# Kernel optimization log

Hardware: AMD Instinct MI355X
Metric: run time of the kernel (lower is better)

Reference implementation:

```python
import jax, jax.numpy as jnp
import numpy as np

B, T, D = 32, 512, 768      # batch, n_tokens, input_dim
M, K, R = 2048, 32, 128     # n_mentions, k_retrieval, retrieval_dim
H = 1024                    # hidden_dim
EPS = 1e-12


def _layer_norm(x, scale, bias, eps=EPS):
    mu = jnp.mean(x, axis=-1, keepdims=True)
    var = jnp.mean(jnp.square(x - mu), axis=-1, keepdims=True)
    return (x - mu) * jax.lax.rsqrt(var + eps) * scale + bias


def _mlp_block(x, w1, b1, w2, b2, ln_s, ln_b):
    # Dense -> gelu -> Dense -> residual -> LayerNorm (dropout off, deterministic)
    h = jax.nn.gelu(x @ w1 + b1)
    h = h @ w2 + b2
    return _layer_norm(h + x, ln_s, ln_b)


def setup_inputs() -> dict:
    key = jax.random.key(0)
    ks = jax.random.split(key, 24)
    s = lambda *sh: 1.0 / np.sqrt(sh[0])
    inp = {
        'encoded_input': jax.random.normal(ks[0], (B, T, D), jnp.float32),
        'retrieval_values': jax.random.normal(ks[1], (M, K, R), jnp.float32),
        'retrieval_scores': jax.random.uniform(ks[2], (M, K), jnp.float32),
        'mention_batch_positions': jax.random.randint(ks[3], (M,), 0, B),
        'mention_start_positions': jax.random.randint(ks[4], (M,), 0, T),
        'mention_end_positions': jax.random.randint(ks[5], (M,), 0, T),
        'mention_mask': jnp.ones((M,), jnp.float32),
        # value_projection: concat(start,end) [2D] -> R
        'vp_w': jax.random.normal(ks[6], (2 * D, R), jnp.float32) * s(2 * D),
        'vp_b': jnp.zeros((R,), jnp.float32),
        # concat_mlp: [2R] -> H ; concat_dense: H -> D
        'cm_w': jax.random.normal(ks[7], (2 * R, H), jnp.float32) * s(2 * R),
        'cm_b': jnp.zeros((H,), jnp.float32),
        'cd_w': jax.random.normal(ks[8], (H, D), jnp.float32) * s(H),
        'cd_b': jnp.zeros((D,), jnp.float32),
        # additional concat MLPBlock (1 layer)
        'ac_w1': jax.random.normal(ks[9], (D, H), jnp.float32) * s(D),
        'ac_b1': jnp.zeros((H,), jnp.float32),
        'ac_w2': jax.random.normal(ks[10], (H, D), jnp.float32) * s(H),
        'ac_b2': jnp.zeros((D,), jnp.float32),
        'ac_ln_s': jnp.ones((D,), jnp.float32),
        'ac_ln_b': jnp.zeros((D,), jnp.float32),
        # pooled MLPBlock (1 layer)
        'pl_w1': jax.random.normal(ks[11], (D, H), jnp.float32) * s(D),
        'pl_b1': jnp.zeros((H,), jnp.float32),
        'pl_w2': jax.random.normal(ks[12], (H, D), jnp.float32) * s(H),
        'pl_b2': jnp.zeros((D,), jnp.float32),
        'pl_ln_s': jnp.ones((D,), jnp.float32),
        'pl_ln_b': jnp.zeros((D,), jnp.float32),
        # final layer norm
        'ln_s': jnp.ones((D,), jnp.float32),
        'ln_b': jnp.zeros((D,), jnp.float32),
    }
    return inp


def reference(encoded_input, retrieval_values, retrieval_scores,
              mention_batch_positions, mention_start_positions,
              mention_end_positions, mention_mask,
              vp_w, vp_b, cm_w, cm_b, cd_w, cd_b,
              ac_w1, ac_b1, ac_w2, ac_b2, ac_ln_s, ac_ln_b,
              pl_w1, pl_b1, pl_w2, pl_b2, pl_ln_s, pl_ln_b,
              ln_s, ln_b):
    # gather mention start/end encodings: [M, D] each
    start_enc = encoded_input[mention_batch_positions, mention_start_positions]
    end_enc = encoded_input[mention_batch_positions, mention_end_positions]
    pmv = jnp.concatenate((start_enc, end_enc), axis=-1) @ vp_w + vp_b  # [M, R]
    # tile over retrievals and concat: [M, K, 2R]
    pmv = jnp.broadcast_to(pmv[:, None, :], (pmv.shape[0], retrieval_values.shape[1], pmv.shape[-1]))
    cv = jnp.concatenate((pmv, retrieval_values), axis=-1)
    cv = jax.nn.gelu(cv @ cm_w + cm_b)
    cv = cv @ cd_w + cd_b                                              # [M, K, D]
    cv = _mlp_block(cv, ac_w1, ac_b1, ac_w2, ac_b2, ac_ln_s, ac_ln_b)
    pooled = jnp.einsum('qk,qkd->qd', retrieval_scores, cv)            # [M, D]
    pooled = _mlp_block(pooled, pl_w1, pl_b1, pl_w2, pl_b2, pl_ln_s, pl_ln_b)
    pooled = pooled * mention_mask[:, None]
    out = encoded_input.at[mention_batch_positions, mention_start_positions].add(pooled)
    return _layer_norm(out, ln_s, ln_b)
```

## Files before the change

### kernel.cpp

```cpp
#include <hip/hip_runtime.h>
#include <hip/hip_bf16.h>

#define Bq 32
#define Tq 512
#define Dq 768
#define Mq 2048
#define Kq 32
#define Rq 128
#define Hq 1024
#define NROWS (Mq * Kq)
#define CH 32768
#define NCH (NROWS / CH)

typedef short short8 __attribute__((ext_vector_type(8)));
typedef unsigned short ushort4v __attribute__((ext_vector_type(4)));
typedef float f32x4 __attribute__((ext_vector_type(4)));

__device__ __forceinline__ unsigned short f2bf(float f) {
    union { float f; unsigned u; } v; v.f = f;
    unsigned r = v.u + 0x7FFFu + ((v.u >> 16) & 1u);
    return (unsigned short)(r >> 16);
}
__device__ __forceinline__ float bf2f(unsigned short h) {
    union { unsigned u; float f; } v; v.u = ((unsigned)h) << 16;
    return v.f;
}
__device__ __forceinline__ float gelu_f(float x) {
    float u = x * (1.5957691216057308f + 0.07135481622212034f * x * x);
    return x / (1.0f + __expf(-u));
}

__device__ __forceinline__ void block_reduce2(float& a, float& b, float* sm) {
    #pragma unroll
    for (int off = 32; off > 0; off >>= 1) {
        a += __shfl_down(a, off, 64);
        b += __shfl_down(b, off, 64);
    }
    int lane = threadIdx.x & 63, wid = threadIdx.x >> 6;
    if (lane == 0) { sm[wid * 2] = a; sm[wid * 2 + 1] = b; }
    __syncthreads();
    if (threadIdx.x == 0) {
        float sa = 0.f, sb = 0.f;
        #pragma unroll
        for (int w = 0; w < 4; ++w) { sa += sm[w * 2]; sb += sm[w * 2 + 1]; }
        sm[0] = sa; sm[1] = sb;
    }
    __syncthreads();
    a = sm[0]; b = sm[1];
    __syncthreads();
}

__global__ __launch_bounds__(256) void wtrans_k(
    const float* __restrict__ W, unsigned short* __restrict__ Wt, int K, int N)
{
    __shared__ unsigned short t[32][33];
    int n0 = blockIdx.x * 32, k0 = blockIdx.y * 32;
    int tx = threadIdx.x & 31, ty = threadIdx.x >> 5;
    #pragma unroll
    for (int i = 0; i < 32; i += 8)
        t[ty + i][tx] = f2bf(W[(long)(k0 + ty + i) * N + n0 + tx]);
    __syncthreads();
    #pragma unroll
    for (int i = 0; i < 32; i += 8)
        Wt[(long)(n0 + ty + i) * K + k0 + tx] = t[tx][ty + i];
}

__global__ __launch_bounds__(256) void rv2bf_k(
    const float* __restrict__ rv, unsigned short* __restrict__ rvb)
{
    long i = ((long)blockIdx.x * 256 + threadIdx.x) * 8;
    float4 a = *reinterpret_cast<const float4*>(rv + i);
    float4 b = *reinterpret_cast<const float4*>(rv + i + 4);
    unsigned short v[8] = {f2bf(a.x), f2bf(a.y), f2bf(a.z), f2bf(a.w),
                           f2bf(b.x), f2bf(b.y), f2bf(b.z), f2bf(b.w)};
    *(short8*)(rvb + i) = *(short8*)v;
}

__global__ __launch_bounds__(192) void gather_enc_k(
    const float* __restrict__ enc, const int* __restrict__ bpos,
    const int* __restrict__ spos, const int* __restrict__ epos,
    unsigned short* __restrict__ cat)
{
    int m = blockIdx.x;
    int t = threadIdx.x;
    int b = bpos[m];
    int pos = (t < 96) ? spos[m] : epos[m];
    int off = (t < 96) ? t * 8 : (t - 96) * 8;
    const float4* s = reinterpret_cast<const float4*>(enc + ((long)b * Tq + pos) * Dq + off);
    float4 a = s[0], c = s[1];
    unsigned short v[8] = {f2bf(a.x), f2bf(a.y), f2bf(a.z), f2bf(a.w),
                           f2bf(c.x), f2bf(c.y), f2bf(c.z), f2bf(c.w)};
    *(short8*)(cat + (long)m * 1536 + t * 8) = *(short8*)v;
}

template <int ACT, int OUT_BF16, int RESID, int CONCAT>
__global__ __launch_bounds__(256) void mgemm_k(
    const unsigned short* __restrict__ A,
    const unsigned short* __restrict__ Wt,
    const float* __restrict__ bias,
    void* __restrict__ Cout,
    const unsigned short* __restrict__ resid,
    int Kd, int N,
    const unsigned short* __restrict__ pmvb,
    const unsigned short* __restrict__ rvb,
    int row_base)
{
    __shared__ __align__(16) unsigned short AsLin[2][128 * 32];
    __shared__ __align__(16) unsigned short BsLin[2][128 * 32];
    const int tid = threadIdx.x;
    const int w = tid >> 6, lane = tid & 63;
    const int wr = w >> 1, wc = w & 1;
    const int lr = lane & 15, lk = lane >> 4;
    const long r0 = (long)blockIdx.x * 128;
    const int c0 = blockIdx.y * 128;
    const int nt = Kd >> 5;

    auto stage = [&](int buf, int t) {
        const int k0 = t << 5;
        #pragma unroll
        for (int cc = 0; cc < 2; ++cc) {
            int idx = (w * 2 + cc) * 64 + lane;
            int row = idx >> 2, kc = idx & 3;
            int kcol = k0 + kc * 8;
            const unsigned short* ga;
            if (CONCAT) {
                long gr = row_base + r0 + row;
                ga = (kcol < 128) ? pmvb + ((gr >> 5) << 7) + kcol
                                  : rvb + (gr << 7) + (kcol - 128);
            } else {
                ga = A + (r0 + row) * Kd + kcol;
            }
            __builtin_amdgcn_global_load_lds(
                (const __attribute__((address_space(1))) void*)ga,
                (__attribute__((address_space(3))) void*)(&AsLin[buf][(w * 2 + cc) * 512]),
                16, 0, 0);
            const unsigned short* gb = Wt + (long)(c0 + row) * Kd + kcol;
            __builtin_amdgcn_global_load_lds(
                (const __attribute__((address_space(1))) void*)gb,
                (__attribute__((address_space(3))) void*)(&BsLin[buf][(w * 2 + cc) * 512]),
                16, 0, 0);
        }
    };

    f32x4 acc[4][4] = {};

    stage(0, 0);
    if (nt > 1) stage(1, 1);

    for (int t = 0; t < nt; ++t) {
        const int cur = t & 1;
        if (t + 1 < nt) asm volatile("s_waitcnt vmcnt(4)" ::: "memory");
        else            asm volatile("s_waitcnt vmcnt(0)" ::: "memory");
        asm volatile("s_barrier" ::: "memory");

        short8 af[4], bv[4];
        #pragma unroll
        for (int m = 0; m < 4; ++m)
            af[m] = *(const short8*)(&AsLin[cur][(wr * 64 + m * 16 + lr) * 32 + lk * 8]);
        #pragma unroll
        for (int n = 0; n < 4; ++n)
            bv[n] = *(const short8*)(&BsLin[cur][(wc * 64 + n * 16 + lr) * 32 + lk * 8]);

        asm volatile("s_waitcnt lgkmcnt(0)" ::: "memory");
        asm volatile("s_barrier" ::: "memory");

        if (t + 2 < nt) stage(cur, t + 2);

        #pragma unroll
        for (int m = 0; m < 4; ++m)
            #pragma unroll
            for (int n = 0; n < 4; ++n)
                acc[m][n] = __builtin_amdgcn_mfma_f32_16x16x32_bf16(
                    af[m], bv[n], acc[m][n], 0, 0, 0);
    }

    const int cb = c0 + wc * 64;
    #pragma unroll
    for (int n = 0; n < 4; ++n) {
        const int c = cb + n * 16 + lr;
        const float bc = bias[c];
        #pragma unroll
        for (int m = 0; m < 4; ++m) {
            const long r = r0 + wr * 64 + m * 16 + lk * 4;
            #pragma unroll
            for (int j = 0; j < 4; ++j) {
                float v = acc[m][n][j] + bc;
                if (ACT) v = gelu_f(v);
                if (RESID) v += bf2f(resid[(r + j) * N + c]);
                if (OUT_BF16) ((unsigned short*)Cout)[(r + j) * N + c] = f2bf(v);
                else          ((float*)Cout)[(r + j) * N + c] = v;
            }
        }
    }
}

template <int ACT, int OUT_BF16, int RESID, int CONCAT, int NF>
__global__ __launch_bounds__(512, 2) void mgemm256_k(
    const unsigned short* __restrict__ A,
    const unsigned short* __restrict__ Wt,
    const float* __restrict__ bias,
    void* __restrict__ Cout,
    const unsigned short* __restrict__ resid,
    int Kd, int N,
    const unsigned short* __restrict__ pmvb,
    const unsigned short* __restrict__ rvb,
    int row_base)
{
    __shared__ __align__(16) unsigned short As[2][256 * 32];
    __shared__ __align__(16) unsigned short Bs[2][NF * 64 * 32];
    const int tid = threadIdx.x;
    const int w = tid >> 6, lane = tid & 63;
    const int wr = w >> 2, wc = w & 3;
    const int lr = lane & 15, lk = lane >> 4;
    const long r0 = (long)blockIdx.x * 256;
    const int c0 = blockIdx.y * (NF * 64);
    const int nt = Kd >> 5;
    const int wb = (NF == 4) ? w : (w >= 6 ? w - 6 : w);

    auto stage = [&](int buf, int t) {
        const int k0 = t << 5;
        #pragma unroll
        for (int q = 0; q < 2; ++q) {
            int ca = w * 128 + q * 64 + lane;
            int rowa = ca >> 2, kca = ca & 3;
            int kcol = k0 + kca * 8;
            const unsigned short* ga;
            if (CONCAT) {
                long gr = row_base + r0 + rowa;
                ga = (kcol < 128) ? pmvb + ((gr >> 5) << 7) + kcol
                                  : rvb + (gr << 7) + (kcol - 128);
            } else {
                ga = A + (r0 + rowa) * Kd + kcol;
            }
            __builtin_amdgcn_global_load_lds(
                (const __attribute__((address_space(1))) void*)ga,
                (__attribute__((address_space(3))) void*)(&As[buf][(w * 128 + q * 64) * 8]),
                16, 0, 0);
            int cb_ = wb * 128 + q * 64 + lane;
            int rowb = cb_ >> 2, kcb = cb_ & 3;
            const unsigned short* gb = Wt + (long)(c0 + rowb) * Kd + k0 + kcb * 8;
            __builtin_amdgcn_global_load_lds(
                (const __attribute__((address_space(1))) void*)gb,
                (__attribute__((address_space(3))) void*)(&Bs[buf][(wb * 128 + q * 64) * 8]),
                16, 0, 0);
        }
    };

    f32x4 acc[8][NF] = {};

    stage(0, 0);
    if (nt > 1) stage(1, 1);

    for (int t = 0; t < nt; ++t) {
        const int cur = t & 1;
        if (t + 1 < nt) asm volatile("s_waitcnt vmcnt(4)" ::: "memory");
        else            asm volatile("s_waitcnt vmcnt(0)" ::: "memory");
        asm volatile("s_barrier" ::: "memory");

        short8 af[8], bv[NF];
        #pragma unroll
        for (int m = 0; m < 8; ++m)
            af[m] = *(const short8*)(&As[cur][(wr * 128 + m * 16 + lr) * 32 + lk * 8]);
        #pragma unroll
        for (int n = 0; n < NF; ++n)
            bv[n] = *(const short8*)(&Bs[cur][(wc * (NF * 16) + n * 16 + lr) * 32 + lk * 8]);

        asm volatile("s_waitcnt lgkmcnt(0)" ::: "memory");
        asm volatile("s_barrier" ::: "memory");

        if (t + 2 < nt) stage(cur, t + 2);

        #pragma unroll
        for (int m = 0; m < 8; ++m)
            #pragma unroll
            for (int n = 0; n < NF; ++n)
                acc[m][n] = __builtin_amdgcn_mfma_f32_16x16x32_bf16(
                    af[m], bv[n], acc[m][n], 0, 0, 0);
    }

    const int cb = c0 + wc * (NF * 16);
    #pragma unroll
    for (int n = 0; n < NF; ++n) {
        const int c = cb + n * 16 + lr;
        const float bc = bias[c];
        #pragma unroll
        for (int m = 0; m < 8; ++m) {
            const long r = r0 + wr * 128 + m * 16 + lk * 4;
            #pragma unroll
            for (int j = 0; j < 4; ++j) {
                float v = acc[m][n][j] + bc;
                if (ACT) v = gelu_f(v);
                if (RESID) v += bf2f(resid[(r + j) * N + c]);
                if (OUT_BF16) ((unsigned short*)Cout)[(r + j) * N + c] = f2bf(v);
                else          ((float*)Cout)[(r + j) * N + c] = v;
            }
        }
    }
}

__global__ __launch_bounds__(512) void ln_pool_part_k(
    const unsigned short* __restrict__ cvb, const float* __restrict__ scores,
    const float* __restrict__ ln_s, const float* __restrict__ ln_b,
    float* __restrict__ partial,
    int mbase)
{
    __shared__ float part[8][768];
    int lm = blockIdx.x >> 2, ks = blockIdx.x & 3;
    int gm = mbase + lm;
    int tid = threadIdx.x, lane = tid & 63, wid = tid >> 6;
    int k = ks * 8 + wid;
    const unsigned short* row = cvb + ((long)lm * 32 + k) * Dq;

    float v[12], gs[12], gb[12];
    float s = 0.f, ss = 0.f;
    #pragma unroll
    for (int j = 0; j < 3; ++j) {
        int col = j * 256 + lane * 4;
        ushort4v u = *(const ushort4v*)(row + col);
        float4 g = *reinterpret_cast<const float4*>(ln_s + col);
        float4 h = *reinterpret_cast<const float4*>(ln_b + col);
        #pragma unroll
        for (int t = 0; t < 4; ++t) {
            float x = bf2f(u[t]);
            v[j * 4 + t] = x;
            s += x; ss += x * x;
        }
        gs[j * 4 + 0] = g.x; gs[j * 4 + 1] = g.y; gs[j * 4 + 2] = g.z; gs[j * 4 + 3] = g.w;
        gb[j * 4 + 0] = h.x; gb[j * 4 + 1] = h.y; gb[j * 4 + 2] = h.z; gb[j * 4 + 3] = h.w;
    }
    #pragma unroll
    for (int off = 32; off > 0; off >>= 1) {
        s  += __shfl_xor(s, off, 64);
        ss += __shfl_xor(ss, off, 64);
    }
    float mu = s * (1.0f / Dq);
    float var = ss * (1.0f / Dq) - mu * mu;
    float rstd = rsqrtf(var + 1e-12f);
    float sc = scores[gm * 32 + k];
    #pragma unroll
    for (int j = 0; j < 3; ++j) {
        int col = j * 256 + lane * 4;
        #pragma unroll
        for (int t = 0; t < 4; ++t)
            part[wid][col + t] = sc * ((v[j * 4 + t] - mu) * rstd * gs[j * 4 + t] + gb[j * 4 + t]);
    }
    __syncthreads();
    for (int d = tid; d < Dq; d += 512) {
        float acc = 0.f;
        #pragma unroll
        for (int w = 0; w < 8; ++w) acc += part[w][d];
        partial[((long)lm * 4 + ks) * Dq + d] = acc;
    }
}

__global__ __launch_bounds__(256) void ln_pool_comb_k(
    const float* __restrict__ partial, float* __restrict__ pooledf,
    unsigned short* __restrict__ pooledb, int mbase)
{
    int lm = blockIdx.x, gm = mbase + lm;
    int tid = threadIdx.x;
    for (int d = tid; d < Dq; d += 256) {
        const float* p = partial + (long)lm * 4 * Dq + d;
        float s = p[0] + p[Dq] + p[2 * Dq] + p[3 * Dq];
        pooledf[(long)gm * Dq + d] = s;
        pooledb[(long)gm * Dq + d] = f2bf(s);
    }
}

__global__ __launch_bounds__(256) void ln_mask_scatter_k(
    const float* __restrict__ pu, const float* __restrict__ pooled,
    const float* __restrict__ ln_s, const float* __restrict__ ln_b,
    const float* __restrict__ mask,
    const int* __restrict__ bpos, const int* __restrict__ spos,
    float* __restrict__ out)
{
    __shared__ float sm[8];
    int m = blockIdx.x;
    int tid = threadIdx.x;
    float v[3];
    float s = 0.f, ss = 0.f;
    #pragma unroll
    for (int j = 0; j < 3; ++j) {
        int d = tid + j * 256;
        v[j] = pu[(long)m * Dq + d] + pooled[(long)m * Dq + d];
        s += v[j]; ss += v[j] * v[j];
    }
    block_reduce2(s, ss, sm);
    float mu = s * (1.0f / Dq);
    float var = ss * (1.0f / Dq) - mu * mu;
    float rstd = rsqrtf(var + 1e-12f);
    float mk = mask[m];
    long orow = ((long)bpos[m] * Tq + spos[m]) * Dq;
    #pragma unroll
    for (int j = 0; j < 3; ++j) {
        int d = tid + j * 256;
        float y = ((v[j] - mu) * rstd * ln_s[d] + ln_b[d]) * mk;
        atomicAdd(&out[orow + d], y);
    }
}

__global__ __launch_bounds__(256) void final_ln_k(
    float* __restrict__ out, const float* __restrict__ ln_s,
    const float* __restrict__ ln_b)
{
    __shared__ float sm[8];
    int tid = threadIdx.x;
    float* row = out + (long)blockIdx.x * Dq;
    float v[3];
    float s = 0.f, ss = 0.f;
    #pragma unroll
    for (int j = 0; j < 3; ++j) {
        v[j] = row[tid + j * 256];
        s += v[j]; ss += v[j] * v[j];
    }
    block_reduce2(s, ss, sm);
    float mu = s * (1.0f / Dq);
    float var = ss * (1.0f / Dq) - mu * mu;
    float rstd = rsqrtf(var + 1e-12f);
    #pragma unroll
    for (int j = 0; j < 3; ++j) {
        int d = tid + j * 256;
        row[d] = (v[j] - mu) * rstd * ln_s[d] + ln_b[d];
    }
}

extern "C" void kernel_launch(void* const* d_in, const int* in_sizes, int n_in,
                              void* d_out, int out_size, void* d_ws, size_t ws_size,
                              hipStream_t stream) {
    const float* enc    = (const float*)d_in[0];
    const float* rv     = (const float*)d_in[1];
    const float* scores = (const float*)d_in[2];
    const int*   bpos   = (const int*)d_in[3];
    const int*   spos   = (const int*)d_in[4];
    const int*   epos   = (const int*)d_in[5];
    const float* mask   = (const float*)d_in[6];
    const float* vp_w   = (const float*)d_in[7];
    const float* vp_b   = (const float*)d_in[8];
    const float* cm_w   = (const float*)d_in[9];
    const float* cm_b   = (const float*)d_in[10];
    const float* cd_w   = (const float*)d_in[11];
    const float* cd_b   = (const float*)d_in[12];
    const float* ac_w1  = (const float*)d_in[13];
    const float* ac_b1  = (const float*)d_in[14];
    const float* ac_w2  = (const float*)d_in[15];
    const float* ac_b2  = (const float*)d_in[16];
    const float* ac_ln_s = (const float*)d_in[17];
    const float* ac_ln_b = (const float*)d_in[18];
    const float* pl_w1  = (const float*)d_in[19];
    const float* pl_b1  = (const float*)d_in[20];
    const float* pl_w2  = (const float*)d_in[21];
    const float* pl_b2  = (const float*)d_in[22];
    const float* pl_ln_s = (const float*)d_in[23];
    const float* pl_ln_b = (const float*)d_in[24];
    const float* ln_s   = (const float*)d_in[25];
    const float* ln_b   = (const float*)d_in[26];
    float* out = (float*)d_out;

    char* wsb = (char*)d_ws;
    unsigned short* wt_cm = (unsigned short*)wsb; wsb += (size_t)1024 * 256 * 2;
    unsigned short* wt_cd = (unsigned short*)wsb; wsb += (size_t)768 * 1024 * 2;
    unsigned short* wt_a1 = (unsigned short*)wsb; wsb += (size_t)1024 * 768 * 2;
    unsigned short* wt_a2 = (unsigned short*)wsb; wsb += (size_t)768 * 1024 * 2;
    unsigned short* wt_p1 = (unsigned short*)wsb; wsb += (size_t)1024 * 768 * 2;
    unsigned short* wt_p2 = (unsigned short*)wsb; wsb += (size_t)768 * 1024 * 2;
    unsigned short* wt_vp = (unsigned short*)wsb; wsb += (size_t)128 * 1536 * 2;
    unsigned short* pmvb  = (unsigned short*)wsb; wsb += (size_t)Mq * Rq * 2;
    unsigned short* rvb   = (unsigned short*)wsb; wsb += (size_t)NROWS * Rq * 2;
    unsigned short* catenc = (unsigned short*)wsb; wsb += (size_t)Mq * 1536 * 2;
    unsigned short* hb    = (unsigned short*)wsb; wsb += (size_t)CH * Hq * 2;
    unsigned short* tb    = (unsigned short*)wsb; wsb += (size_t)CH * Dq * 2;
    unsigned short* cvb   = (unsigned short*)wsb; wsb += (size_t)CH * Dq * 2;
    float* partial = (float*)wsb; wsb += (size_t)(CH / Kq) * 4 * Dq * 4;
    float* pooledf = (float*)wsb; wsb += (size_t)Mq * Dq * 4;
    unsigned short* pooledb = (unsigned short*)wsb; wsb += (size_t)Mq * Dq * 2;
    float* puf     = (float*)wsb; wsb += (size_t)Mq * Dq * 4;

    hipMemcpyAsync(out, enc, (size_t)Bq * Tq * Dq * sizeof(float),
                   hipMemcpyDeviceToDevice, stream);

    wtrans_k<<<dim3(1024 / 32, 256 / 32), 256, 0, stream>>>(cm_w, wt_cm, 256, 1024);
    wtrans_k<<<dim3(768 / 32, 1024 / 32), 256, 0, stream>>>(cd_w, wt_cd, 1024, 768);
    wtrans_k<<<dim3(1024 / 32, 768 / 32), 256, 0, stream>>>(ac_w1, wt_a1, 768, 1024);
    wtrans_k<<<dim3(768 / 32, 1024 / 32), 256, 0, stream>>>(ac_w2, wt_a2, 1024, 768);
    wtrans_k<<<dim3(1024 / 32, 768 / 32), 256, 0, stream>>>(pl_w1, wt_p1, 768, 1024);
    wtrans_k<<<dim3(768 / 32, 1024 / 32), 256, 0, stream>>>(pl_w2, wt_p2, 1024, 768);
    wtrans_k<<<dim3(128 / 32, 1536 / 32), 256, 0, stream>>>(vp_w, wt_vp, 1536, 128);
    rv2bf_k<<<(NROWS * Rq) / (256 * 8), 256, 0, stream>>>(rv, rvb);

    gather_enc_k<<<Mq, 192, 0, stream>>>(enc, bpos, spos, epos, catenc);
    mgemm_k<0, 1, 0, 0><<<dim3(Mq / 128, 1), 256, 0, stream>>>(
        catenc, wt_vp, vp_b, pmvb, nullptr, 1536, Rq, nullptr, nullptr, 0);

    for (int c = 0; c < NCH; ++c) {
        int row_base = c * CH;
        int mbase = c * (CH / Kq);
        mgemm256_k<1, 1, 0, 1, 4><<<dim3(CH / 256, Hq / 256), 512, 0, stream>>>(
            nullptr, wt_cm, cm_b, hb, nullptr, 2 * Rq, Hq, pmvb, rvb, row_base);
        mgemm256_k<0, 1, 0, 0, 3><<<dim3(CH / 256, Dq / 192), 512, 0, stream>>>(
            hb, wt_cd, cd_b, tb, nullptr, Hq, Dq, nullptr, nullptr, 0);
        mgemm256_k<1, 1, 0, 0, 4><<<dim3(CH / 256, Hq / 256), 512, 0, stream>>>(
            tb, wt_a1, ac_b1, hb, nullptr, Dq, Hq, nullptr, nullptr, 0);
        mgemm256_k<0, 1, 1, 0, 3><<<dim3(CH / 256, Dq / 192), 512, 0, stream>>>(
            hb, wt_a2, ac_b2, cvb, tb, Hq, Dq, nullptr, nullptr, 0);
        ln_pool_part_k<<<(CH / Kq) * 4, 512, 0, stream>>>(
            cvb, scores, ac_ln_s, ac_ln_b, partial, mbase);
        ln_pool_comb_k<<<CH / Kq, 256, 0, stream>>>(partial, pooledf, pooledb, mbase);
    }

    mgemm_k<1, 1, 0, 0><<<dim3(Mq / 128, Hq / 128), 256, 0, stream>>>(
        pooledb, wt_p1, pl_b1, hb, nullptr, Dq, Hq, nullptr, nullptr, 0);
    mgemm_k<0, 0, 0, 0><<<dim3(Mq / 128, Dq / 128), 256, 0, stream>>>(
        hb, wt_p2, pl_b2, puf, nullptr, Hq, Dq, nullptr, nullptr, 0);

    ln_mask_scatter_k<<<Mq, 256, 0, stream>>>(puf, pooledf, pl_ln_s, pl_ln_b,
                                              mask, bpos, spos, out);

    final_ln_k<<<Bq * Tq, 256, 0, stream>>>(out, ln_s, ln_b);
}
```

Before: 795.1 us.

## Split GEMM k-step MFMAs around barrier, add XCD-aware block swizzle

```diff
diff --git a/kernel.cpp b/kernel.cpp
--- a/kernel.cpp
+++ b/kernel.cpp
@@ -194,7 +194,7 @@
     }
 }
 
-template <int ACT, int OUT_BF16, int RESID, int CONCAT, int NF>
+template <int ACT, int OUT_BF16, int RESID, int CONCAT>
 __global__ __launch_bounds__(512, 2) void mgemm256_k(
     const unsigned short* __restrict__ A,
     const unsigned short* __restrict__ Wt,
@@ -207,15 +207,22 @@
     int row_base)
 {
     __shared__ __align__(16) unsigned short As[2][256 * 32];
-    __shared__ __align__(16) unsigned short Bs[2][NF * 64 * 32];
+    __shared__ __align__(16) unsigned short Bs[2][256 * 32];
     const int tid = threadIdx.x;
     const int w = tid >> 6, lane = tid & 63;
     const int wr = w >> 2, wc = w & 3;
     const int lr = lane & 15, lk = lane >> 4;
-    const long r0 = (long)blockIdx.x * 256;
-    const int c0 = blockIdx.y * (NF * 64);
+
+    const int rows = gridDim.x, cols = gridDim.y;
+    const int lin = blockIdx.x + blockIdx.y * rows;
+    const int xcd = lin & 7, s = lin >> 3;
+    const int rpx = rows >> 3;
+    const int bcol = s % cols;
+    const int brow = xcd * rpx + s / cols;
+
+    const long r0 = (long)brow * 256;
+    const int c0 = bcol * 256;
     const int nt = Kd >> 5;
-    const int wb = (NF == 4) ? w : (w >= 6 ? w - 6 : w);
 
     auto stage = [&](int buf, int t) {
         const int k0 = t << 5;
@@ -236,17 +243,15 @@
                 (const __attribute__((address_space(1))) void*)ga,
                 (__attribute__((address_space(3))) void*)(&As[buf][(w * 128 + q * 64) * 8]),
                 16, 0, 0);
-            int cb_ = wb * 128 + q * 64 + lane;
-            int rowb = cb_ >> 2, kcb = cb_ & 3;
-            const unsigned short* gb = Wt + (long)(c0 + rowb) * Kd + k0 + kcb * 8;
+            const unsigned short* gb = Wt + (long)(c0 + rowa) * Kd + kcol;
             __builtin_amdgcn_global_load_lds(
                 (const __attribute__((address_space(1))) void*)gb,
-                (__attribute__((address_space(3))) void*)(&Bs[buf][(wb * 128 + q * 64) * 8]),
+                (__attribute__((address_space(3))) void*)(&Bs[buf][(w * 128 + q * 64) * 8]),
                 16, 0, 0);
         }
     };
 
-    f32x4 acc[8][NF] = {};
+    f32x4 acc[8][4] = {};
 
     stage(0, 0);
     if (nt > 1) stage(1, 1);
@@ -257,30 +262,47 @@
         else            asm volatile("s_waitcnt vmcnt(0)" ::: "memory");
         asm volatile("s_barrier" ::: "memory");
 
-        short8 af[8], bv[NF];
-        #pragma unroll
-        for (int m = 0; m < 8; ++m)
-            af[m] = *(const short8*)(&As[cur][(wr * 128 + m * 16 + lr) * 32 + lk * 8]);
-        #pragma unroll
-        for (int n = 0; n < NF; ++n)
-            bv[n] = *(const short8*)(&Bs[cur][(wc * (NF * 16) + n * 16 + lr) * 32 + lk * 8]);
+        short8 af0[4], af1[4], bv[4];
+        #pragma unroll
+        for (int m = 0; m < 4; ++m)
+            af0[m] = *(const short8*)(&As[cur][(wr * 128 + m * 16 + lr) * 32 + lk * 8]);
+        #pragma unroll
+        for (int n = 0; n < 4; ++n)
+            bv[n] = *(const short8*)(&Bs[cur][(wc * 64 + n * 16 + lr) * 32 + lk * 8]);
+        asm volatile("s_waitcnt lgkmcnt(0)" ::: "memory");
+
+        #pragma unroll
+        for (int m = 0; m < 4; ++m)
+            af1[m] = *(const short8*)(&As[cur][(wr * 128 + (m + 4) * 16 + lr) * 32 + lk * 8]);
+        __builtin_amdgcn_sched_barrier(0);
+
+        __builtin_amdgcn_s_setprio(1);
+        #pragma unroll
+        for (int m = 0; m < 4; ++m)
+            #pragma unroll
+            for (int n = 0; n < 4; ++n)
+                acc[m][n] = __builtin_amdgcn_mfma_f32_16x16x32_bf16(
+                    af0[m], bv[n], acc[m][n], 0, 0, 0);
+        __builtin_amdgcn_s_setprio(0);
 
         asm volatile("s_waitcnt lgkmcnt(0)" ::: "memory");
         asm volatile("s_barrier" ::: "memory");
 
         if (t + 2 < nt) stage(cur, t + 2);
 
-        #pragma unroll
-        for (int m = 0; m < 8; ++m)
+        __builtin_amdgcn_s_setprio(1);
+        #pragma unroll
+        for (int m = 0; m < 4; ++m)
             #pragma unroll
-            for (int n = 0; n < NF; ++n)
-                acc[m][n] = __builtin_amdgcn_mfma_f32_16x16x32_bf16(
-                    af[m], bv[n], acc[m][n], 0, 0, 0);
-    }
-
-    const int cb = c0 + wc * (NF * 16);
-    #pragma unroll
-    for (int n = 0; n < NF; ++n) {
+            for (int n = 0; n < 4; ++n)
+                acc[m + 4][n] = __builtin_amdgcn_mfma_f32_16x16x32_bf16(
+                    af1[m], bv[n], acc[m + 4][n], 0, 0, 0);
+        __builtin_amdgcn_s_setprio(0);
+    }
+
+    const int cb = c0 + wc * 64;
+    #pragma unroll
+    for (int n = 0; n < 4; ++n) {
         const int c = cb + n * 16 + lr;
         const float bc = bias[c];
         #pragma unroll
@@ -494,13 +516,13 @@
     for (int c = 0; c < NCH; ++c) {
         int row_base = c * CH;
         int mbase = c * (CH / Kq);
-        mgemm256_k<1, 1, 0, 1, 4><<<dim3(CH / 256, Hq / 256), 512, 0, stream>>>(
+        mgemm256_k<1, 1, 0, 1><<<dim3(CH / 256, Hq / 256), 512, 0, stream>>>(
             nullptr, wt_cm, cm_b, hb, nullptr, 2 * Rq, Hq, pmvb, rvb, row_base);
-        mgemm256_k<0, 1, 0, 0, 3><<<dim3(CH / 256, Dq / 192), 512, 0, stream>>>(
+        mgemm256_k<0, 1, 0, 0><<<dim3(CH / 256, Dq / 256), 512, 0, stream>>>(
             hb, wt_cd, cd_b, tb, nullptr, Hq, Dq, nullptr, nullptr, 0);
-        mgemm256_k<1, 1, 0, 0, 4><<<dim3(CH / 256, Hq / 256), 512, 0, stream>>>(
+        mgemm256_k<1, 1, 0, 0><<<dim3(CH / 256, Hq / 256), 512, 0, stream>>>(
             tb, wt_a1, ac_b1, hb, nullptr, Dq, Hq, nullptr, nullptr, 0);
-        mgemm256_k<0, 1, 1, 0, 3><<<dim3(CH / 256, Dq / 192), 512, 0, stream>>>(
+        mgemm256_k<0, 1, 1, 0><<<dim3(CH / 256, Dq / 256), 512, 0, stream>>>(
             hb, wt_a2, ac_b2, cvb, tb, Hq, Dq, nullptr, nullptr, 0);
         ln_pool_part_k<<<(CH / Kq) * 4, 512, 0, stream>>>(
             cvb, scores, ac_ln_s, ac_ln_b, partial, mbase);
```

New measurement: 840.0 us. 5.6% more time.

## Restructure big GEMM with 64-wide K tiles, swizzled LDS, XCD remap and ping-pong schedule

Applied to the files above, without the earlier changes.

```diff
diff --git a/kernel.cpp b/kernel.cpp
--- a/kernel.cpp
+++ b/kernel.cpp
@@ -195,7 +195,7 @@
 }
 
 template <int ACT, int OUT_BF16, int RESID, int CONCAT, int NF>
-__global__ __launch_bounds__(512, 2) void mgemm256_k(
+__global__ __launch_bounds__(512, 1) void mg8_k(
     const unsigned short* __restrict__ A,
     const unsigned short* __restrict__ Wt,
     const float* __restrict__ bias,
@@ -206,76 +206,154 @@
     const unsigned short* __restrict__ rvb,
     int row_base)
 {
-    __shared__ __align__(16) unsigned short As[2][256 * 32];
-    __shared__ __align__(16) unsigned short Bs[2][NF * 64 * 32];
+    __shared__ __align__(16) unsigned short As[2][256 * 64];
+    __shared__ __align__(16) unsigned short Bs[2][NF * 64 * 64];
     const int tid = threadIdx.x;
     const int w = tid >> 6, lane = tid & 63;
     const int wr = w >> 2, wc = w & 3;
     const int lr = lane & 15, lk = lane >> 4;
-    const long r0 = (long)blockIdx.x * 256;
-    const int c0 = blockIdx.y * (NF * 64);
-    const int nt = Kd >> 5;
-    const int wb = (NF == 4) ? w : (w >= 6 ? w - 6 : w);
-
-    auto stage = [&](int buf, int t) {
-        const int k0 = t << 5;
-        #pragma unroll
-        for (int q = 0; q < 2; ++q) {
-            int ca = w * 128 + q * 64 + lane;
-            int rowa = ca >> 2, kca = ca & 3;
-            int kcol = k0 + kca * 8;
+
+    const int rows = gridDim.x, cols = gridDim.y;
+    const int lin = blockIdx.x + blockIdx.y * rows;
+    const int xcd = lin & 7, sq = lin >> 3;
+    const int rpx = rows >> 3;
+    const int bcol = sq % cols;
+    const int brow = xcd * rpx + sq / cols;
+
+    const long r0 = (long)brow * 256;
+    const int c0 = bcol * (NF * 64);
+    const int nt = Kd >> 6;
+    const int swz = (lr & 7) << 3;
+
+    auto stageA = [&](int buf, int t) {
+        #pragma unroll
+        for (int q = 0; q < 4; ++q) {
+            int idx = q * 512 + tid;
+            int row = idx >> 3;
+            int slot = (idx & 7) ^ (row & 7);
+            int gk = (t << 6) + slot * 8;
             const unsigned short* ga;
             if (CONCAT) {
-                long gr = row_base + r0 + rowa;
-                ga = (kcol < 128) ? pmvb + ((gr >> 5) << 7) + kcol
-                                  : rvb + (gr << 7) + (kcol - 128);
+                long gr = row_base + r0 + row;
+                ga = (gk < 128) ? pmvb + ((gr >> 5) << 7) + gk
+                                : rvb + (gr << 7) + (gk - 128);
             } else {
-                ga = A + (r0 + rowa) * Kd + kcol;
+                ga = A + (r0 + row) * Kd + gk;
             }
             __builtin_amdgcn_global_load_lds(
                 (const __attribute__((address_space(1))) void*)ga,
-                (__attribute__((address_space(3))) void*)(&As[buf][(w * 128 + q * 64) * 8]),
+                (__attribute__((address_space(3))) void*)(&As[buf][idx * 8]),
                 16, 0, 0);
-            int cb_ = wb * 128 + q * 64 + lane;
-            int rowb = cb_ >> 2, kcb = cb_ & 3;
-            const unsigned short* gb = Wt + (long)(c0 + rowb) * Kd + k0 + kcb * 8;
+        }
+    };
+    auto stageB = [&](int buf, int t) {
+        #pragma unroll
+        for (int q = 0; q < NF; ++q) {
+            int idx = q * 512 + tid;
+            int row = idx >> 3;
+            int slot = (idx & 7) ^ (row & 7);
+            int gk = (t << 6) + slot * 8;
+            const unsigned short* gb = Wt + (long)(c0 + row) * Kd + gk;
             __builtin_amdgcn_global_load_lds(
                 (const __attribute__((address_space(1))) void*)gb,
-                (__attribute__((address_space(3))) void*)(&Bs[buf][(wb * 128 + q * 64) * 8]),
+                (__attribute__((address_space(3))) void*)(&Bs[buf][idx * 8]),
                 16, 0, 0);
         }
     };
 
     f32x4 acc[8][NF] = {};
 
-    stage(0, 0);
-    if (nt > 1) stage(1, 1);
+    stageA(0, 0); stageB(0, 0);
+    stageA(1, 1); stageB(1, 1);
+    if (NF == 4) asm volatile("s_waitcnt vmcnt(8)" ::: "memory");
+    else         asm volatile("s_waitcnt vmcnt(7)" ::: "memory");
+    asm volatile("s_barrier" ::: "memory");
 
     for (int t = 0; t < nt; ++t) {
         const int cur = t & 1;
-        if (t + 1 < nt) asm volatile("s_waitcnt vmcnt(4)" ::: "memory");
-        else            asm volatile("s_waitcnt vmcnt(0)" ::: "memory");
-        asm volatile("s_barrier" ::: "memory");
-
-        short8 af[8], bv[NF];
-        #pragma unroll
-        for (int m = 0; m < 8; ++m)
-            af[m] = *(const short8*)(&As[cur][(wr * 128 + m * 16 + lr) * 32 + lk * 8]);
-        #pragma unroll
-        for (int n = 0; n < NF; ++n)
-            bv[n] = *(const short8*)(&Bs[cur][(wc * (NF * 16) + n * 16 + lr) * 32 + lk * 8]);
-
+        const bool do_stage = (t >= 1) && (t + 1 < nt);
+        short8 af[4], bv0[NF], bv1[NF];
+
+        #pragma unroll
+        for (int mm = 0; mm < 4; ++mm) {
+            int row = wr * 128 + mm * 16 + lr;
+            af[mm] = *(const short8*)(&As[cur][row * 64 + ((lk * 8) ^ swz)]);
+        }
+        #pragma unroll
+        for (int n = 0; n < NF; ++n) {
+            int row = wc * (NF * 16) + n * 16 + lr;
+            bv0[n] = *(const short8*)(&Bs[cur][row * 64 + ((lk * 8) ^ swz)]);
+        }
+        if (do_stage) stageA(cur ^ 1, t + 1);
+        asm volatile("s_barrier" ::: "memory");
         asm volatile("s_waitcnt lgkmcnt(0)" ::: "memory");
-        asm volatile("s_barrier" ::: "memory");
-
-        if (t + 2 < nt) stage(cur, t + 2);
-
-        #pragma unroll
-        for (int m = 0; m < 8; ++m)
+        __builtin_amdgcn_s_setprio(1);
+        #pragma unroll
+        for (int mm = 0; mm < 4; ++mm)
             #pragma unroll
             for (int n = 0; n < NF; ++n)
-                acc[m][n] = __builtin_amdgcn_mfma_f32_16x16x32_bf16(
-                    af[m], bv[n], acc[m][n], 0, 0, 0);
+                acc[mm][n] = __builtin_amdgcn_mfma_f32_16x16x32_bf16(
+                    af[mm], bv0[n], acc[mm][n], 0, 0, 0);
+        __builtin_amdgcn_s_setprio(0);
+        asm volatile("s_barrier" ::: "memory");
+
+        #pragma unroll
+        for (int mm = 0; mm < 4; ++mm) {
+            int row = wr * 128 + 64 + mm * 16 + lr;
+            af[mm] = *(const short8*)(&As[cur][row * 64 + ((lk * 8) ^ swz)]);
+        }
+        if (do_stage) stageB(cur ^ 1, t + 1);
+        asm volatile("s_barrier" ::: "memory");
+        asm volatile("s_waitcnt lgkmcnt(0)" ::: "memory");
+        __builtin_amdgcn_s_setprio(1);
+        #pragma unroll
+        for (int mm = 0; mm < 4; ++mm)
+            #pragma unroll
+            for (int n = 0; n < NF; ++n)
+                acc[4 + mm][n] = __builtin_amdgcn_mfma_f32_16x16x32_bf16(
+                    af[mm], bv0[n], acc[4 + mm][n], 0, 0, 0);
+        __builtin_amdgcn_s_setprio(0);
+        asm volatile("s_barrier" ::: "memory");
+
+        #pragma unroll
+        for (int mm = 0; mm < 4; ++mm) {
+            int row = wr * 128 + mm * 16 + lr;
+            af[mm] = *(const short8*)(&As[cur][row * 64 + ((32 + lk * 8) ^ swz)]);
+        }
+        #pragma unroll
+        for (int n = 0; n < NF; ++n) {
+            int row = wc * (NF * 16) + n * 16 + lr;
+            bv1[n] = *(const short8*)(&Bs[cur][row * 64 + ((32 + lk * 8) ^ swz)]);
+        }
+        asm volatile("s_barrier" ::: "memory");
+        asm volatile("s_waitcnt lgkmcnt(0)" ::: "memory");
+        __builtin_amdgcn_s_setprio(1);
+        #pragma unroll
+        for (int mm = 0; mm < 4; ++mm)
+            #pragma unroll
+            for (int n = 0; n < NF; ++n)
+                acc[mm][n] = __builtin_amdgcn_mfma_f32_16x16x32_bf16(
+                    af[mm], bv1[n], acc[mm][n], 0, 0, 0);
+        __builtin_amdgcn_s_setprio(0);
+        asm volatile("s_barrier" ::: "memory");
+
+        #pragma unroll
+        for (int mm = 0; mm < 4; ++mm) {
+            int row = wr * 128 + 64 + mm * 16 + lr;
+            af[mm] = *(const short8*)(&As[cur][row * 64 + ((32 + lk * 8) ^ swz)]);
+        }
+        asm volatile("s_barrier" ::: "memory");
+        asm volatile("s_waitcnt lgkmcnt(0)" ::: "memory");
+        __builtin_amdgcn_s_setprio(1);
+        #pragma unroll
+        for (int mm = 0; mm < 4; ++mm)
+            #pragma unroll
+            for (int n = 0; n < NF; ++n)
+                acc[4 + mm][n] = __builtin_amdgcn_mfma_f32_16x16x32_bf16(
+                    af[mm], bv1[n], acc[4 + mm][n], 0, 0, 0);
+        __builtin_amdgcn_s_setprio(0);
+        if (t + 1 < nt) asm volatile("s_waitcnt vmcnt(0)" ::: "memory");
+        asm volatile("s_barrier" ::: "memory");
     }
 
     const int cb = c0 + wc * (NF * 16);
@@ -494,13 +572,13 @@
     for (int c = 0; c < NCH; ++c) {
         int row_base = c * CH;
         int mbase = c * (CH / Kq);
-        mgemm256_k<1, 1, 0, 1, 4><<<dim3(CH / 256, Hq / 256), 512, 0, stream>>>(
+        mg8_k<1, 1, 0, 1, 4><<<dim3(CH / 256, Hq / 256), 512, 0, stream>>>(
             nullptr, wt_cm, cm_b, hb, nullptr, 2 * Rq, Hq, pmvb, rvb, row_base);
-        mgemm256_k<0, 1, 0, 0, 3><<<dim3(CH / 256, Dq / 192), 512, 0, stream>>>(
+        mg8_k<0, 1, 0, 0, 3><<<dim3(CH / 256, Dq / 192), 512, 0, stream>>>(
             hb, wt_cd, cd_b, tb, nullptr, Hq, Dq, nullptr, nullptr, 0);
-        mgemm256_k<1, 1, 0, 0, 4><<<dim3(CH / 256, Hq / 256), 512, 0, stream>>>(
+        mg8_k<1, 1, 0, 0, 4><<<dim3(CH / 256, Hq / 256), 512, 0, stream>>>(
             tb, wt_a1, ac_b1, hb, nullptr, Dq, Hq, nullptr, nullptr, 0);
-        mgemm256_k<0, 1, 1, 0, 3><<<dim3(CH / 256, Dq / 192), 512, 0, stream>>>(
+        mg8_k<0, 1, 1, 0, 3><<<dim3(CH / 256, Dq / 192), 512, 0, stream>>>(
             hb, wt_a2, ac_b2, cvb, tb, Hq, Dq, nullptr, nullptr, 0);
         ln_pool_part_k<<<(CH / Kq) * 4, 512, 0, stream>>>(
             cvb, scores, ac_ln_s, ac_ln_b, partial, mbase);
```

Measured after the change: 714.5 us. 1.11x faster.
